# Optimization experiments

Hardware: AMD Instinct MI355X
Metric: run time of the kernel (lower is better)

The kernel has to match this reference:

```python
import jax, jax.numpy as jnp
import numpy as np

N = 50000
E = 500000
IN_DIM = 128
HID = 128
EDGE_DIM = 1
MAX_DEPTH = 4  # depth values in [0, MAX_DEPTH]


def setup_inputs() -> dict:
    key = jax.random.key(0)
    ks = jax.random.split(key, 10)
    x = jax.random.normal(ks[0], (N, IN_DIM), jnp.float32)
    edge_index = jax.random.randint(ks[1], (2, E), 0, N)
    edge_attr = jax.random.normal(ks[2], (E, EDGE_DIM), jnp.float32)
    depth = jax.random.randint(ks[3], (N,), 0, MAX_DEPTH + 1)
    def w(k, sh):
        return (jax.random.normal(k, sh, jnp.float32) / np.float32(np.sqrt(sh[0])))
    return {
        "x": x, "edge_index": edge_index, "edge_attr": edge_attr, "depth": depth,
        "pw": w(ks[4], (IN_DIM, HID)), "pb": jnp.zeros((HID,), jnp.float32),
        "mw1": w(ks[5], (HID + EDGE_DIM, HID)), "mb1": jnp.zeros((HID,), jnp.float32),
        "mw2": w(ks[6], (HID, HID)), "mb2": jnp.zeros((HID,), jnp.float32),
        "uw1": w(ks[7], (2 * HID, HID)), "ub1": jnp.zeros((HID,), jnp.float32),
        "uw2": w(ks[8], (HID, HID)), "ub2": jnp.zeros((HID,), jnp.float32),
    }


def reference(x, edge_index, edge_attr, depth, pw, pb, mw1, mb1, mw2, mb2, uw1, ub1, uw2, ub2):
    src, dst = edge_index[0], edge_index[1]
    dst_depth = depth[dst]  # [E]
    h = x @ pw + pb  # node_proj -> [N, HID]
    # Sequential topological DP over depth levels (static unroll, small count).
    for d in range(1, MAX_DEPTH + 1):
        emask = dst_depth == d  # [E]
        # msg_mlp over all edges using current h (lower-depth nodes already updated)
        msg_in = jnp.concatenate([h[src], edge_attr], axis=-1)  # [E, HID+EDGE_DIM]
        msgs = jax.nn.relu(jax.nn.relu(msg_in @ mw1 + mb1) @ mw2 + mb2)
        msgs = jnp.where(emask[:, None], msgs, jnp.zeros((), h.dtype))
        agg = jax.ops.segment_sum(msgs, dst, num_segments=N)  # [N, HID]
        counts = jax.ops.segment_sum(emask.astype(h.dtype), dst, num_segments=N)
        agg = agg / jnp.clip(counts, 1.0)[:, None]  # mean aggregation, clamp(min=1)
        upd_in = jnp.concatenate([h, agg], axis=-1)  # [N, 2*HID]
        h_new = jax.nn.relu(jax.nn.relu(upd_in @ uw1 + ub1) @ uw2 + ub2)
        h = jnp.where((depth == d)[:, None], h_new, h)
    return h
```

## Files before the change

### kernel.cpp

```cpp
#include <hip/hip_runtime.h>

typedef _Float16 f16;
typedef f16 f16x2 __attribute__((ext_vector_type(2)));
typedef f16 f16x8 __attribute__((ext_vector_type(8)));
typedef float f32x4 __attribute__((ext_vector_type(4)));
typedef float f32x2 __attribute__((ext_vector_type(2)));

#define MFMA16(a, b, c) __builtin_amdgcn_mfma_f32_16x16x32_f16((a), (b), (c), 0, 0, 0)

static __device__ __forceinline__ f16x8 cvt8(const float* __restrict__ p) {
    f32x4 p0 = *(const f32x4*)p;
    f32x4 p1 = *(const f32x4*)(p + 4);
    f16x8 a;
    a[0] = (f16)p0[0]; a[1] = (f16)p0[1]; a[2] = (f16)p0[2]; a[3] = (f16)p0[3];
    a[4] = (f16)p1[0]; a[5] = (f16)p1[1]; a[6] = (f16)p1[2]; a[7] = (f16)p1[3];
    return a;
}

__global__ __launch_bounds__(256) void k_prep(
        const float* __restrict__ pw, const float* __restrict__ mw1,
        const float* __restrict__ mw2, const float* __restrict__ uw1,
        const float* __restrict__ uw2,
        f16* __restrict__ pwp, f16* __restrict__ mw1p, f16* __restrict__ mw2p,
        f16* __restrict__ uw1p, f16* __restrict__ uw2p,
        const int* __restrict__ ei, int* __restrict__ degv,
        const int* __restrict__ dep, int* __restrict__ dcnt,
        int4* __restrict__ recs, int CB, int E, int N) {
    __shared__ int lcnt[4];
    __shared__ int lbase[4];
    int b = blockIdx.x;
    int t = threadIdx.x;
    if (b < 48) {
        const float* W; f16* out; int fb;
        if (b < 8)       { W = pw;  out = pwp;  fb = b; }
        else if (b < 16) { W = mw1; out = mw1p; fb = b - 8; }
        else if (b < 24) { W = mw2; out = mw2p; fb = b - 16; }
        else if (b < 40) { W = uw1; out = uw1p; fb = b - 24; }
        else             { W = uw2; out = uw2p; fb = b - 40; }
        int idx = fb * 256 + t;
        int lane = idx & 63;
        int nt = (idx >> 6) & 7;
        int kt = idx >> 9;
        int colx = lane & 15, quad = lane >> 4;
        f16* o = out + (size_t)idx * 8;
        const float* wb = W + (size_t)(kt * 32 + quad * 8) * 128 + nt * 16 + colx;
#pragma unroll
        for (int j = 0; j < 8; j++) o[j] = (f16)wb[(size_t)j * 128];
    } else if (b < 48 + CB) {
        int e = (b - 48) * 256 + t;
        if (e < E) atomicAdd(&degv[ei[E + e]], 1);
    } else {
        if (t < 4) lcnt[t] = 0;
        __syncthreads();
        int v = (b - 48 - CB) * 256 + t;
        int d = (v < N) ? dep[v] : 0;
        int p = -1;
        if (d >= 1 && d <= 4) p = atomicAdd(&lcnt[d - 1], 1);
        __syncthreads();
        if (t < 4) lbase[t] = (lcnt[t] > 0) ? atomicAdd(&dcnt[t], lcnt[t]) : 0;
        __syncthreads();
        if (d >= 1 && d <= 4) recs[(size_t)(d - 1) * N + lbase[d - 1] + p].x = v;
    }
}

__global__ __launch_bounds__(256) void k_mid(
        const int* __restrict__ degv, int* __restrict__ bsum, int SB,
        const float* __restrict__ x, const f16* __restrict__ pwp,
        const f16* __restrict__ mw1p, const float* __restrict__ pb,
        const float* __restrict__ mb1, float* __restrict__ h,
        f16* __restrict__ hh, f16* __restrict__ t, int N) {
    __shared__ __align__(16) f16 lds[4][16 * 136];
    __shared__ int wsum[4];
    int tid = threadIdx.x;
    if ((int)blockIdx.x < SB) {
        int idx = blockIdx.x * 256 + tid;
        int v = (idx < N) ? degv[idx] : 0;
#pragma unroll
        for (int off = 32; off; off >>= 1) v += __shfl_down(v, off, 64);
        if ((tid & 63) == 0) wsum[tid >> 6] = v;
        __syncthreads();
        if (tid == 0) bsum[blockIdx.x] = wsum[0] + wsum[1] + wsum[2] + wsum[3];
        return;
    }
    int lane = tid & 63, w = tid >> 6;
    int colx = lane & 15, quad = lane >> 4;
    int base = ((blockIdx.x - SB) * 4 + w) * 16;
    int arow = base + colx;
    int u = arow < N ? arow : N - 1;

    f32x4 c1[8];
#pragma unroll
    for (int nt = 0; nt < 8; nt++) c1[nt] = (f32x4){0.f, 0.f, 0.f, 0.f};
#pragma unroll
    for (int kt = 0; kt < 4; kt++) {
        f16x8 a = cvt8(x + (size_t)u * 128 + kt * 32 + quad * 8);
#pragma unroll
        for (int nt = 0; nt < 8; nt++) {
            f16x8 b = *(const f16x8*)(pwp + ((size_t)(kt * 8 + nt) * 64 + lane) * 8);
            c1[nt] = MFMA16(a, b, c1[nt]);
        }
    }
#pragma unroll
    for (int nt = 0; nt < 8; nt++) {
        float bias = pb[nt * 16 + colx];
#pragma unroll
        for (int reg = 0; reg < 4; reg++) {
            int row = quad * 4 + reg;
            int node = base + row;
            float v = c1[nt][reg] + bias;
            lds[w][row * 136 + nt * 16 + colx] = (f16)v;
            if (node < N) {
                h[(size_t)node * 128 + nt * 16 + colx] = v;
                hh[(size_t)node * 128 + nt * 16 + colx] = (f16)v;
            }
        }
    }
    f32x4 c2[8];
#pragma unroll
    for (int nt = 0; nt < 8; nt++) c2[nt] = (f32x4){0.f, 0.f, 0.f, 0.f};
#pragma unroll
    for (int kt = 0; kt < 4; kt++) {
        f16x8 a = *(const f16x8*)&lds[w][colx * 136 + kt * 32 + quad * 8];
#pragma unroll
        for (int nt = 0; nt < 8; nt++) {
            f16x8 b = *(const f16x8*)(mw1p + ((size_t)(kt * 8 + nt) * 64 + lane) * 8);
            c2[nt] = MFMA16(a, b, c2[nt]);
        }
    }
#pragma unroll
    for (int nt = 0; nt < 8; nt++) {
        float bias = mb1[nt * 16 + colx];
#pragma unroll
        for (int reg = 0; reg < 4; reg++) {
            int node = base + quad * 4 + reg;
            if (node < N) t[(size_t)node * 128 + nt * 16 + colx] = (f16)(c2[nt][reg] + bias);
        }
    }
}

__global__ __launch_bounds__(256) void k_scanC(const int* __restrict__ degv,
                                               const int* __restrict__ bsum,
                                               int* __restrict__ rowp, int N, int E) {
    __shared__ int lds[256];
    __shared__ int wo[4];
    int b = blockIdx.x, t = threadIdx.x;
    int idx = b * 256 + t;
    int v = (idx < N) ? degv[idx] : 0;
    lds[t] = v;
    __syncthreads();
#pragma unroll
    for (int d = 1; d < 256; d <<= 1) {
        int u = (t >= d) ? lds[t - d] : 0;
        __syncthreads();
        lds[t] += u;
        __syncthreads();
    }
    int off = 0;
    for (int j = t; j < b; j += 256) off += bsum[j];
#pragma unroll
    for (int o = 32; o; o >>= 1) off += __shfl_down(off, o, 64);
    if ((t & 63) == 0) wo[t >> 6] = off;
    __syncthreads();
    int boff = wo[0] + wo[1] + wo[2] + wo[3];
    if (idx < N) rowp[idx] = boff + lds[t] - v;
    if (b == 0 && t == 0) rowp[N] = E;
}

__global__ __launch_bounds__(256) void k_scat(const int* __restrict__ ei,
                                              const float* __restrict__ eattr,
                                              const int* __restrict__ rowp,
                                              int* __restrict__ cur,
                                              int2* __restrict__ esea,
                                              int4* __restrict__ recs,
                                              const int* __restrict__ dcnt,
                                              int E, int N) {
    int gtid = blockIdx.x * 256 + threadIdx.x;
    int gsz = gridDim.x * 256;
    for (int e = gtid; e < E; e += gsz) {
        int s = ei[e], d = ei[E + e];
        int p = rowp[d] + atomicAdd(&cur[d], 1);
        esea[p] = (int2){s, __float_as_int(eattr[e])};
    }
    for (int d4 = 0; d4 < 4; d4++) {
        int cnt = dcnt[d4];
        for (int i = gtid; i < cnt; i += gsz) {
            int4* r = &recs[(size_t)d4 * N + i];
            int u = r->x;
            r->y = rowp[u];
            r->z = rowp[u + 1];
        }
    }
}

__global__ __launch_bounds__(256) void k_m(
        const f16* __restrict__ t, const float* __restrict__ mw1,
        const float* __restrict__ mb2, const f16* __restrict__ mw2p,
        const int2* __restrict__ esea,
        const int4* __restrict__ recs, const int* __restrict__ dcnt,
        int dIdx, f16* __restrict__ agg, int N) {
    __shared__ __align__(16) f16 bsm[128 * 128];
    {
        const f16x8* s8 = (const f16x8*)mw2p;
        f16x8* d8 = (f16x8*)bsm;
        for (int i = threadIdx.x; i < 2048; i += 256) d8[i] = s8[i];
    }
    __syncthreads();

    const int tid = threadIdx.x;
    const int lane = tid & 63;
    const int colx = lane & 15, quad = lane >> 4;
    const int gwv = blockIdx.x * 4 + (tid >> 6), nwv = gridDim.x * 4;
    const int cnt = dcnt[dIdx];

    const float* w1r = mw1 + 128 * 128;
    f16x8 w1h[4];
#pragma unroll
    for (int kt = 0; kt < 4; kt++) {
        f32x4 q0 = *(const f32x4*)(w1r + kt * 32 + quad * 8);
        f32x4 q1 = *(const f32x4*)(w1r + kt * 32 + quad * 8 + 4);
        w1h[kt][0] = (f16)q0[0]; w1h[kt][1] = (f16)q0[1];
        w1h[kt][2] = (f16)q0[2]; w1h[kt][3] = (f16)q0[3];
        w1h[kt][4] = (f16)q1[0]; w1h[kt][5] = (f16)q1[1];
        w1h[kt][6] = (f16)q1[2]; w1h[kt][7] = (f16)q1[3];
    }
    float mb2v[8];
#pragma unroll
    for (int nt = 0; nt < 8; nt++) mb2v[nt] = mb2[nt * 16 + colx];

    struct Pre { int u, e0, e1; f16 eah; f16x8 tv[4]; };
    auto load_pre = [&](int n) {
        Pre p;
        int4 r = recs[(size_t)dIdx * N + n];
        p.u = r.x; p.e0 = r.y; p.e1 = r.z;
        int lim = p.e1 - 1; if (lim < 0) lim = 0;
        int es = p.e0 + colx; if (es > lim) es = lim;
        int2 er = esea[es];
        p.eah = (f16)__int_as_float(er.y);
        const f16* trow = t + (size_t)er.x * 128;
#pragma unroll
        for (int kt = 0; kt < 4; kt++)
            p.tv[kt] = *(const f16x8*)(trow + kt * 32 + quad * 8);
        return p;
    };
    auto build_afr = [&](const f16x8* tv, f16 eah, f16x8* afr) {
#pragma unroll
        for (int kt = 0; kt < 4; kt++) {
            f16x8 v = tv[kt];
            f16x8 o;
#pragma unroll
            for (int j = 0; j < 8; j++) {
                f16 q = v[j] + eah * w1h[kt][j];
                o[j] = q > (f16)0 ? q : (f16)0;
            }
            afr[kt] = o;
        }
    };
    auto tile_acc = [&](f16x8* afr, int bs, int e1, float* aggv) {
#pragma unroll
        for (int nt = 0; nt < 8; nt++) {
            f32x4 c = (f32x4){0.f, 0.f, 0.f, 0.f};
#pragma unroll
            for (int kt = 0; kt < 4; kt++) {
                f16x8 b = *(const f16x8*)&bsm[((kt * 8 + nt) * 64 + lane) * 8];
                c = MFMA16(afr[kt], b, c);
            }
#pragma unroll
            for (int reg = 0; reg < 4; reg++)
                if (bs + quad * 4 + reg < e1) aggv[nt] += fmaxf(c[reg] + mb2v[nt], 0.f);
        }
    };
    auto process = [&](const Pre& p) {
        float aggv[8] = {0.f, 0.f, 0.f, 0.f, 0.f, 0.f, 0.f, 0.f};
        f16x8 afr[4];
        build_afr(p.tv, p.eah, afr);
        tile_acc(afr, p.e0, p.e1, aggv);
        for (int bs = p.e0 + 16; bs < p.e1; bs += 16) {
            int lim = p.e1 - 1;
            int es = bs + colx; if (es > lim) es = lim;
            int2 er = esea[es];
            f16 eah = (f16)__int_as_float(er.y);
            const f16* trow = t + (size_t)er.x * 128;
            f16x8 tv[4];
#pragma unroll
            for (int kt = 0; kt < 4; kt++)
                tv[kt] = *(const f16x8*)(trow + kt * 32 + quad * 8);
            build_afr(tv, eah, afr);
            tile_acc(afr, bs, p.e1, aggv);
        }
        int deg = p.e1 - p.e0;
        float inv = 1.f / (float)(deg > 1 ? deg : 1);
#pragma unroll
        for (int nt = 0; nt < 8; nt++) {
            float s = aggv[nt];
            s += __shfl_xor(s, 16, 64);
            s += __shfl_xor(s, 32, 64);
            if (quad == 0) agg[(size_t)p.u * 128 + nt * 16 + colx] = (f16)(s * inv);
        }
    };
    int stride2 = nwv * 2;
    for (int base = gwv * 2; base < cnt; base += stride2) {
        Pre p0 = load_pre(base);
        bool has1 = (base + 1) < cnt;
        if (has1) {
            Pre p1 = load_pre(base + 1);
            process(p0);
            process(p1);
        } else {
            process(p0);
        }
    }
}

__global__ __launch_bounds__(256) void k_u(
        float* h, f16* t, const f16* __restrict__ hh, const f16* __restrict__ agg,
        const f16* __restrict__ uw1p, const f16* __restrict__ uw2p,
        const f16* __restrict__ mw1p,
        const float* __restrict__ ub1, const float* __restrict__ ub2,
        const float* __restrict__ mb1,
        const int4* __restrict__ recs, const int* __restrict__ dcnt,
        int dIdx, int N) {
    __shared__ __align__(16) f16 shb[4][2][16 * 136];
    const int tid = threadIdx.x;
    const int lane = tid & 63, w = tid >> 6;
    const int colx = lane & 15, quad = lane >> 4;
    const int gwv = blockIdx.x * 4 + w, nwv = gridDim.x * 4;
    const int cnt = dcnt[dIdx];
    const int ntiles = (cnt + 15) >> 4;

    for (int tb = gwv; tb < ntiles; tb += nwv) {
        int base = tb * 16;
        int aidx = base + colx;
        int ua = (aidx < cnt) ? recs[(size_t)dIdx * N + aidx].x : 0;
        int un[4];
        bool uvalid[4];
#pragma unroll
        for (int reg = 0; reg < 4; reg++) {
            int node = base + quad * 4 + reg;
            uvalid[reg] = node < cnt;
            un[reg] = uvalid[reg] ? recs[(size_t)dIdx * N + node].x : 0;
        }

        f32x4 c1[8];
#pragma unroll
        for (int nt = 0; nt < 8; nt++) c1[nt] = (f32x4){0.f, 0.f, 0.f, 0.f};
#pragma unroll
        for (int kt = 0; kt < 8; kt++) {
            f16x8 a;
            if (kt < 4)
                a = *(const f16x8*)(hh + (size_t)ua * 128 + kt * 32 + quad * 8);
            else
                a = *(const f16x8*)(agg + (size_t)ua * 128 + (kt - 4) * 32 + quad * 8);
#pragma unroll
            for (int nt = 0; nt < 8; nt++) {
                f16x8 b = *(const f16x8*)(uw1p + ((size_t)(kt * 8 + nt) * 64 + lane) * 8);
                c1[nt] = MFMA16(a, b, c1[nt]);
            }
        }
#pragma unroll
        for (int nt = 0; nt < 8; nt++) {
            float bias = ub1[nt * 16 + colx];
#pragma unroll
            for (int reg = 0; reg < 4; reg++) {
                int row = quad * 4 + reg;
                shb[w][0][row * 136 + nt * 16 + colx] = (f16)fmaxf(c1[nt][reg] + bias, 0.f);
            }
        }
        f32x4 c2[8];
#pragma unroll
        for (int nt = 0; nt < 8; nt++) c2[nt] = (f32x4){0.f, 0.f, 0.f, 0.f};
#pragma unroll
        for (int kt = 0; kt < 4; kt++) {
            f16x8 a = *(const f16x8*)&shb[w][0][colx * 136 + kt * 32 + quad * 8];
#pragma unroll
            for (int nt = 0; nt < 8; nt++) {
                f16x8 b = *(const f16x8*)(uw2p + ((size_t)(kt * 8 + nt) * 64 + lane) * 8);
                c2[nt] = MFMA16(a, b, c2[nt]);
            }
        }
#pragma unroll
        for (int nt = 0; nt < 8; nt++) {
            float bias = ub2[nt * 16 + colx];
#pragma unroll
            for (int reg = 0; reg < 4; reg++) {
                int row = quad * 4 + reg;
                float v = fmaxf(c2[nt][reg] + bias, 0.f);
                shb[w][1][row * 136 + nt * 16 + colx] = (f16)v;
                if (uvalid[reg]) h[(size_t)un[reg] * 128 + nt * 16 + colx] = v;
            }
        }
        f32x4 c3[8];
#pragma unroll
        for (int nt = 0; nt < 8; nt++) c3[nt] = (f32x4){0.f, 0.f, 0.f, 0.f};
#pragma unroll
        for (int kt = 0; kt < 4; kt++) {
            f16x8 a = *(const f16x8*)&shb[w][1][colx * 136 + kt * 32 + quad * 8];
#pragma unroll
            for (int nt = 0; nt < 8; nt++) {
                f16x8 b = *(const f16x8*)(mw1p + ((size_t)(kt * 8 + nt) * 64 + lane) * 8);
                c3[nt] = MFMA16(a, b, c3[nt]);
            }
        }
#pragma unroll
        for (int nt = 0; nt < 8; nt++) {
            float bias = mb1[nt * 16 + colx];
#pragma unroll
            for (int reg = 0; reg < 4; reg++) {
                if (uvalid[reg])
                    t[(size_t)un[reg] * 128 + nt * 16 + colx] = (f16)(c3[nt][reg] + bias);
            }
        }
    }
}

extern "C" void kernel_launch(void* const* d_in, const int* in_sizes, int n_in,
                              void* d_out, int out_size, void* d_ws, size_t ws_size,
                              hipStream_t stream) {
    const float* x    = (const float*)d_in[0];
    const int*   ei   = (const int*)d_in[1];
    const float* eatt = (const float*)d_in[2];
    const int*   dep  = (const int*)d_in[3];
    const float* pw   = (const float*)d_in[4];
    const float* pb   = (const float*)d_in[5];
    const float* mw1  = (const float*)d_in[6];
    const float* mb1  = (const float*)d_in[7];
    const float* mw2  = (const float*)d_in[8];
    const float* mb2  = (const float*)d_in[9];
    const float* uw1  = (const float*)d_in[10];
    const float* ub1  = (const float*)d_in[11];
    const float* uw2  = (const float*)d_in[12];
    const float* ub2  = (const float*)d_in[13];
    float* h = (float*)d_out;

    int N = in_sizes[3];
    int E = in_sizes[1] / 2;
    int NB = (N + 255) / 256;
    int CB = (E + 255) / 256;

    char* ws = (char*)d_ws;
    size_t o = 0;
    auto alloc = [&](size_t bytes) -> char* {
        char* p = ws + o;
        o += (bytes + 255) & ~(size_t)255;
        return p;
    };
    f16*   t    = (f16*)alloc((size_t)N * 128 * 2);
    f16*   hh   = (f16*)alloc((size_t)N * 128 * 2);
    f16*   agg  = (f16*)alloc((size_t)N * 128 * 2);
    char*  z0   = (char*)alloc(0);
    int*   degv = (int*)alloc((size_t)N * 4);
    int*   cur  = (int*)alloc((size_t)N * 4);
    int*   dcnt = (int*)alloc(64);
    size_t zbytes = (size_t)((char*)alloc(0) - z0);
    int*   rowp = (int*)alloc((size_t)(N + 1) * 4);
    int*   bsum = (int*)alloc((size_t)NB * 4);
    int2*  esea = (int2*)alloc((size_t)E * 8);
    int4*  recs = (int4*)alloc((size_t)4 * N * 16);
    f16*   pwp  = (f16*)alloc(128 * 128 * 2);
    f16*   mw1p = (f16*)alloc(128 * 128 * 2);
    f16*   mw2p = (f16*)alloc(128 * 128 * 2);
    f16*   uw1p = (f16*)alloc(256 * 128 * 2);
    f16*   uw2p = (f16*)alloc(128 * 128 * 2);

    hipMemsetAsync(z0, 0, zbytes, stream);

    k_prep<<<48 + CB + NB, 256, 0, stream>>>(pw, mw1, mw2, uw1, uw2,
                                             pwp, mw1p, mw2p, uw1p, uw2p,
                                             ei, degv, dep, dcnt, recs, CB, E, N);
    int PB = (N + 63) / 64;
    k_mid<<<NB + PB, 256, 0, stream>>>(degv, bsum, NB, x, pwp, mw1p, pb, mb1,
                                       h, hh, t, N);
    k_scanC<<<NB, 256, 0, stream>>>(degv, bsum, rowp, N, E);
    k_scat<<<CB, 256, 0, stream>>>(ei, eatt, rowp, cur, esea, recs, dcnt, E, N);

    for (int d = 0; d < 4; d++) {
        k_m<<<1024, 256, 0, stream>>>(t, mw1, mb2, mw2p, esea, recs, dcnt,
                                      d, agg, N);
        k_u<<<256, 256, 0, stream>>>(h, t, hh, agg, uw1p, uw2p, mw1p, ub1, ub2,
                                     mb1, recs, dcnt, d, N);
    }
}
```

Baseline: 375.6 us.

## Fuse message aggregation and node update into one per-level kernel

Merges the per-depth message kernel and update kernel into a single kernel. Each block aggregates a chunk of 16 nodes into shared memory, then runs the update MLP and the next-level first-layer projection with the four waves splitting output columns. This removes the agg global round trip and half of the launches. To avoid read/write races on t within one launch, updated projections go to a separate tUpd buffer, and the source depth is packed into the edge record to pick which buffer to read. The cost is extra block barriers, fewer waves working per node tile, and a 20-bit limit on node ids.

After: 348.3 us. -7.3%, faster.

```diff
diff --git a/kernel.cpp b/kernel.cpp
--- a/kernel.cpp
+++ b/kernel.cpp
@@ -168,6 +168,7 @@
 
 __global__ __launch_bounds__(256) void k_scat(const int* __restrict__ ei,
                                               const float* __restrict__ eattr,
+                                              const int* __restrict__ dep,
                                               const int* __restrict__ rowp,
                                               int* __restrict__ cur,
                                               int2* __restrict__ esea,
@@ -179,7 +180,7 @@
     for (int e = gtid; e < E; e += gsz) {
         int s = ei[e], d = ei[E + e];
         int p = rowp[d] + atomicAdd(&cur[d], 1);
-        esea[p] = (int2){s, __float_as_int(eattr[e])};
+        esea[p] = (int2){s | (dep[s] << 20), __float_as_int(eattr[e])};
     }
     for (int d4 = 0; d4 < 4; d4++) {
         int cnt = dcnt[d4];
@@ -192,24 +193,32 @@
     }
 }
 
-__global__ __launch_bounds__(256) void k_m(
-        const f16* __restrict__ t, const float* __restrict__ mw1,
-        const float* __restrict__ mb2, const f16* __restrict__ mw2p,
-        const int2* __restrict__ esea,
+__global__ __launch_bounds__(256) void k_md(
+        const f16* __restrict__ tOrg, f16* __restrict__ tUpd,
+        const float* __restrict__ mw1, const float* __restrict__ mb2,
+        const f16* __restrict__ mw2p, const int2* __restrict__ esea,
         const int4* __restrict__ recs, const int* __restrict__ dcnt,
-        int dIdx, f16* __restrict__ agg, int N) {
+        const f16* __restrict__ hh, const f16* __restrict__ uw1p,
+        const f16* __restrict__ uw2p, const f16* __restrict__ mw1p,
+        const float* __restrict__ ub1, const float* __restrict__ ub2,
+        const float* __restrict__ mb1, float* __restrict__ h,
+        int dIdx, int N) {
     __shared__ __align__(16) f16 bsm[128 * 128];
+    __shared__ __align__(16) f16 pool[16][136];
+    __shared__ __align__(16) f16 sout[16][136];
+    __shared__ int ids[16];
     {
         const f16x8* s8 = (const f16x8*)mw2p;
         f16x8* d8 = (f16x8*)bsm;
         for (int i = threadIdx.x; i < 2048; i += 256) d8[i] = s8[i];
     }
+    if (threadIdx.x < 16) ids[threadIdx.x] = 0;
     __syncthreads();
 
     const int tid = threadIdx.x;
     const int lane = tid & 63;
+    const int w = tid >> 6;
     const int colx = lane & 15, quad = lane >> 4;
-    const int gwv = blockIdx.x * 4 + (tid >> 6), nwv = gridDim.x * 4;
     const int cnt = dcnt[dIdx];
 
     const float* w1r = mw1 + 128 * 128;
@@ -228,6 +237,10 @@
     for (int nt = 0; nt < 8; nt++) mb2v[nt] = mb2[nt * 16 + colx];
 
     struct Pre { int u, e0, e1; f16 eah; f16x8 tv[4]; };
+    auto srow = [&](int sv) -> const f16* {
+        const f16* tb = ((unsigned)((sv >> 20) - 1) < (unsigned)dIdx) ? tUpd : tOrg;
+        return tb + (size_t)(sv & 0xFFFFF) * 128;
+    };
     auto load_pre = [&](int n) {
         Pre p;
         int4 r = recs[(size_t)dIdx * N + n];
@@ -236,7 +249,7 @@
         int es = p.e0 + colx; if (es > lim) es = lim;
         int2 er = esea[es];
         p.eah = (f16)__int_as_float(er.y);
-        const f16* trow = t + (size_t)er.x * 128;
+        const f16* trow = srow(er.x);
 #pragma unroll
         for (int kt = 0; kt < 4; kt++)
             p.tv[kt] = *(const f16x8*)(trow + kt * 32 + quad * 8);
@@ -269,7 +282,7 @@
                 if (bs + quad * 4 + reg < e1) aggv[nt] += fmaxf(c[reg] + mb2v[nt], 0.f);
         }
     };
-    auto process = [&](const Pre& p) {
+    auto process = [&](const Pre& p, int r) {
         float aggv[8] = {0.f, 0.f, 0.f, 0.f, 0.f, 0.f, 0.f, 0.f};
         f16x8 afr[4];
         build_afr(p.tv, p.eah, afr);
@@ -279,7 +292,7 @@
             int es = bs + colx; if (es > lim) es = lim;
             int2 er = esea[es];
             f16 eah = (f16)__int_as_float(er.y);
-            const f16* trow = t + (size_t)er.x * 128;
+            const f16* trow = srow(er.x);
             f16x8 tv[4];
 #pragma unroll
             for (int kt = 0; kt < 4; kt++)
@@ -294,121 +307,111 @@
             float s = aggv[nt];
             s += __shfl_xor(s, 16, 64);
             s += __shfl_xor(s, 32, 64);
-            if (quad == 0) agg[(size_t)p.u * 128 + nt * 16 + colx] = (f16)(s * inv);
-        }
-    };
-    int stride2 = nwv * 2;
-    for (int base = gwv * 2; base < cnt; base += stride2) {
-        Pre p0 = load_pre(base);
-        bool has1 = (base + 1) < cnt;
-        if (has1) {
-            Pre p1 = load_pre(base + 1);
-            process(p0);
-            process(p1);
-        } else {
-            process(p0);
-        }
-    }
-}
-
-__global__ __launch_bounds__(256) void k_u(
-        float* h, f16* t, const f16* __restrict__ hh, const f16* __restrict__ agg,
-        const f16* __restrict__ uw1p, const f16* __restrict__ uw2p,
-        const f16* __restrict__ mw1p,
-        const float* __restrict__ ub1, const float* __restrict__ ub2,
-        const float* __restrict__ mb1,
-        const int4* __restrict__ recs, const int* __restrict__ dcnt,
-        int dIdx, int N) {
-    __shared__ __align__(16) f16 shb[4][2][16 * 136];
-    const int tid = threadIdx.x;
-    const int lane = tid & 63, w = tid >> 6;
-    const int colx = lane & 15, quad = lane >> 4;
-    const int gwv = blockIdx.x * 4 + w, nwv = gridDim.x * 4;
-    const int cnt = dcnt[dIdx];
-    const int ntiles = (cnt + 15) >> 4;
-
-    for (int tb = gwv; tb < ntiles; tb += nwv) {
-        int base = tb * 16;
-        int aidx = base + colx;
-        int ua = (aidx < cnt) ? recs[(size_t)dIdx * N + aidx].x : 0;
-        int un[4];
-        bool uvalid[4];
-#pragma unroll
-        for (int reg = 0; reg < 4; reg++) {
-            int node = base + quad * 4 + reg;
-            uvalid[reg] = node < cnt;
-            un[reg] = uvalid[reg] ? recs[(size_t)dIdx * N + node].x : 0;
-        }
-
-        f32x4 c1[8];
-#pragma unroll
-        for (int nt = 0; nt < 8; nt++) c1[nt] = (f32x4){0.f, 0.f, 0.f, 0.f};
+            if (quad == 0) pool[r][nt * 16 + colx] = (f16)(s * inv);
+        }
+        if (lane == 0) ids[r] = p.u;
+    };
+
+    const int b = blockIdx.x, nb = gridDim.x;
+    const int s0 = (int)((long long)cnt * b / nb);
+    const int s1 = (int)((long long)cnt * (b + 1) / nb);
+
+    for (int cs = s0; cs < s1; cs += 16) {
+        int cc = s1 - cs; if (cc > 16) cc = 16;
+        for (int rr = w; rr < cc; rr += 8) {
+            Pre p0 = load_pre(cs + rr);
+            if (rr + 4 < cc) {
+                Pre p1 = load_pre(cs + rr + 4);
+                process(p0, rr);
+                process(p1, rr + 4);
+            } else {
+                process(p0, rr);
+            }
+        }
+        __syncthreads();
+        int arid = ids[colx];
+        f32x4 c1[2];
+        c1[0] = (f32x4){0.f, 0.f, 0.f, 0.f};
+        c1[1] = (f32x4){0.f, 0.f, 0.f, 0.f};
 #pragma unroll
         for (int kt = 0; kt < 8; kt++) {
             f16x8 a;
             if (kt < 4)
-                a = *(const f16x8*)(hh + (size_t)ua * 128 + kt * 32 + quad * 8);
+                a = *(const f16x8*)(hh + (size_t)arid * 128 + kt * 32 + quad * 8);
             else
-                a = *(const f16x8*)(agg + (size_t)ua * 128 + (kt - 4) * 32 + quad * 8);
-#pragma unroll
-            for (int nt = 0; nt < 8; nt++) {
-                f16x8 b = *(const f16x8*)(uw1p + ((size_t)(kt * 8 + nt) * 64 + lane) * 8);
-                c1[nt] = MFMA16(a, b, c1[nt]);
-            }
-        }
-#pragma unroll
-        for (int nt = 0; nt < 8; nt++) {
+                a = *(const f16x8*)&pool[colx][(kt - 4) * 32 + quad * 8];
+#pragma unroll
+            for (int j = 0; j < 2; j++) {
+                int nt = 2 * w + j;
+                f16x8 bb = *(const f16x8*)(uw1p + ((size_t)(kt * 8 + nt) * 64 + lane) * 8);
+                c1[j] = MFMA16(a, bb, c1[j]);
+            }
+        }
+#pragma unroll
+        for (int j = 0; j < 2; j++) {
+            int nt = 2 * w + j;
             float bias = ub1[nt * 16 + colx];
 #pragma unroll
             for (int reg = 0; reg < 4; reg++) {
                 int row = quad * 4 + reg;
-                shb[w][0][row * 136 + nt * 16 + colx] = (f16)fmaxf(c1[nt][reg] + bias, 0.f);
-            }
-        }
-        f32x4 c2[8];
-#pragma unroll
-        for (int nt = 0; nt < 8; nt++) c2[nt] = (f32x4){0.f, 0.f, 0.f, 0.f};
+                sout[row][nt * 16 + colx] = (f16)fmaxf(c1[j][reg] + bias, 0.f);
+            }
+        }
+        __syncthreads();
+        f32x4 c2[2];
+        c2[0] = (f32x4){0.f, 0.f, 0.f, 0.f};
+        c2[1] = (f32x4){0.f, 0.f, 0.f, 0.f};
 #pragma unroll
         for (int kt = 0; kt < 4; kt++) {
-            f16x8 a = *(const f16x8*)&shb[w][0][colx * 136 + kt * 32 + quad * 8];
-#pragma unroll
-            for (int nt = 0; nt < 8; nt++) {
-                f16x8 b = *(const f16x8*)(uw2p + ((size_t)(kt * 8 + nt) * 64 + lane) * 8);
-                c2[nt] = MFMA16(a, b, c2[nt]);
-            }
-        }
-#pragma unroll
-        for (int nt = 0; nt < 8; nt++) {
+            f16x8 a = *(const f16x8*)&sout[colx][kt * 32 + quad * 8];
+#pragma unroll
+            for (int j = 0; j < 2; j++) {
+                int nt = 2 * w + j;
+                f16x8 bb = *(const f16x8*)(uw2p + ((size_t)(kt * 8 + nt) * 64 + lane) * 8);
+                c2[j] = MFMA16(a, bb, c2[j]);
+            }
+        }
+#pragma unroll
+        for (int j = 0; j < 2; j++) {
+            int nt = 2 * w + j;
             float bias = ub2[nt * 16 + colx];
 #pragma unroll
             for (int reg = 0; reg < 4; reg++) {
                 int row = quad * 4 + reg;
-                float v = fmaxf(c2[nt][reg] + bias, 0.f);
-                shb[w][1][row * 136 + nt * 16 + colx] = (f16)v;
-                if (uvalid[reg]) h[(size_t)un[reg] * 128 + nt * 16 + colx] = v;
-            }
-        }
-        f32x4 c3[8];
-#pragma unroll
-        for (int nt = 0; nt < 8; nt++) c3[nt] = (f32x4){0.f, 0.f, 0.f, 0.f};
-#pragma unroll
-        for (int kt = 0; kt < 4; kt++) {
-            f16x8 a = *(const f16x8*)&shb[w][1][colx * 136 + kt * 32 + quad * 8];
-#pragma unroll
-            for (int nt = 0; nt < 8; nt++) {
-                f16x8 b = *(const f16x8*)(mw1p + ((size_t)(kt * 8 + nt) * 64 + lane) * 8);
-                c3[nt] = MFMA16(a, b, c3[nt]);
-            }
-        }
-#pragma unroll
-        for (int nt = 0; nt < 8; nt++) {
-            float bias = mb1[nt * 16 + colx];
-#pragma unroll
-            for (int reg = 0; reg < 4; reg++) {
-                if (uvalid[reg])
-                    t[(size_t)un[reg] * 128 + nt * 16 + colx] = (f16)(c3[nt][reg] + bias);
-            }
-        }
+                float v = fmaxf(c2[j][reg] + bias, 0.f);
+                pool[row][nt * 16 + colx] = (f16)v;
+                if (row < cc)
+                    h[(size_t)ids[row] * 128 + nt * 16 + colx] = v;
+            }
+        }
+        __syncthreads();
+        if (dIdx < 3) {
+            f32x4 c3[2];
+            c3[0] = (f32x4){0.f, 0.f, 0.f, 0.f};
+            c3[1] = (f32x4){0.f, 0.f, 0.f, 0.f};
+#pragma unroll
+            for (int kt = 0; kt < 4; kt++) {
+                f16x8 a = *(const f16x8*)&pool[colx][kt * 32 + quad * 8];
+#pragma unroll
+                for (int j = 0; j < 2; j++) {
+                    int nt = 2 * w + j;
+                    f16x8 bb = *(const f16x8*)(mw1p + ((size_t)(kt * 8 + nt) * 64 + lane) * 8);
+                    c3[j] = MFMA16(a, bb, c3[j]);
+                }
+            }
+#pragma unroll
+            for (int j = 0; j < 2; j++) {
+                int nt = 2 * w + j;
+                float bias = mb1[nt * 16 + colx];
+#pragma unroll
+                for (int reg = 0; reg < 4; reg++) {
+                    int row = quad * 4 + reg;
+                    if (row < cc)
+                        tUpd[(size_t)ids[row] * 128 + nt * 16 + colx] = (f16)(c3[j][reg] + bias);
+                }
+            }
+        }
+        __syncthreads();
     }
 }
 
@@ -445,7 +448,7 @@
     };
     f16*   t    = (f16*)alloc((size_t)N * 128 * 2);
     f16*   hh   = (f16*)alloc((size_t)N * 128 * 2);
-    f16*   agg  = (f16*)alloc((size_t)N * 128 * 2);
+    f16*   tUpd = (f16*)alloc((size_t)N * 128 * 2);
     char*  z0   = (char*)alloc(0);
     int*   degv = (int*)alloc((size_t)N * 4);
     int*   cur  = (int*)alloc((size_t)N * 4);
@@ -470,12 +473,11 @@
     k_mid<<<NB + PB, 256, 0, stream>>>(degv, bsum, NB, x, pwp, mw1p, pb, mb1,
                                        h, hh, t, N);
     k_scanC<<<NB, 256, 0, stream>>>(degv, bsum, rowp, N, E);
-    k_scat<<<CB, 256, 0, stream>>>(ei, eatt, rowp, cur, esea, recs, dcnt, E, N);
+    k_scat<<<CB, 256, 0, stream>>>(ei, eatt, dep, rowp, cur, esea, recs, dcnt, E, N);
 
     for (int d = 0; d < 4; d++) {
-        k_m<<<1024, 256, 0, stream>>>(t, mw1, mb2, mw2p, esea, recs, dcnt,
-                                      d, agg, N);
-        k_u<<<256, 256, 0, stream>>>(h, t, hh, agg, uw1p, uw2p, mw1p, ub1, ub2,
-                                     mb1, recs, dcnt, d, N);
-    }
-}
+        k_md<<<768, 256, 0, stream>>>(t, tUpd, mw1, mb2, mw2p, esea, recs, dcnt,
+                                      hh, uw1p, uw2p, mw1p, ub1, ub2, mb1, h,
+                                      d, N);
+    }
+}
```
